# Kernel optimization log

Hardware: AMD Instinct MI355X
Metric: run time of the kernel (lower is better)

The kernel has to match this reference:

```python
import jax, jax.numpy as jnp
import numpy as np

HEAD = 4      # args.head
N_HOPS = 2    # n_hops == gt_layer


def setup_inputs() -> dict:
    key = jax.random.key(0)
    ks = jax.random.split(key, 8)
    N, D, E, R = 100000, 64, 800000, 32
    entity_emb = jax.random.normal(ks[0], (N, D), dtype=jnp.float32) * 0.1
    weight = jax.random.normal(ks[1], (R - 1, D), dtype=jnp.float32) * 0.1
    Wq = jax.random.normal(ks[2], (N_HOPS, D, D), dtype=jnp.float32) * (1.0 / np.sqrt(D))
    Wk = jax.random.normal(ks[3], (N_HOPS, D, D), dtype=jnp.float32) * (1.0 / np.sqrt(D))
    Wv = jax.random.normal(ks[4], (N_HOPS, D, D), dtype=jnp.float32) * (1.0 / np.sqrt(D))
    edge_index = jax.random.randint(ks[5], (2, E), 0, N, dtype=jnp.int64 if jax.config.jax_enable_x64 else jnp.int32)
    edge_type = jax.random.randint(ks[6], (E,), 1, R, dtype=edge_index.dtype)  # in [1, R-1]
    return {"entity_emb": entity_emb, "weight": weight, "Wq": Wq, "Wk": Wk,
            "Wv": Wv, "edge_index": edge_index, "edge_type": edge_type}


def _kg_layer(rows, col_embeds, embeds, n_nodes, wq, wk, wv):
    # per-edge scaled-dot attention with index_add softmax normalization
    E, D = col_embeds.shape
    dh = D // HEAD
    q = (embeds[rows] @ wq).reshape(E, HEAD, dh)
    k = (col_embeds @ wk).reshape(E, HEAD, dh)
    v = (col_embeds @ wv).reshape(E, HEAD, dh)
    att = jnp.clip(jnp.einsum('ehd,ehd->eh', q, k), -10.0, 10.0)
    exp_att = jnp.exp(att)                                        # [E, H]
    att_norm = jax.ops.segment_sum(exp_att, rows, num_segments=n_nodes)[rows]
    a = exp_att / (att_norm + 1e-8)
    res = (a[..., None] * v).reshape(E, D)
    return jax.ops.segment_sum(res, rows, num_segments=n_nodes)   # [N, D]


def _scatter_softmax(x, index, n_seg):
    # numerically-stable softmax over edges grouped by index (torch_scatter.scatter_softmax)
    m = jax.ops.segment_max(x, index, num_segments=n_seg)
    e = jnp.exp(x - m[index])
    s = jax.ops.segment_sum(e, index, num_segments=n_seg)
    return e / (s[index] + 1e-16)


def reference(entity_emb, weight, Wq, Wk, Wv, edge_index, edge_type):
    N, D = entity_emb.shape
    head, tail = edge_index[0], edge_index[1]
    rel = weight[edge_type - 1]                                   # [E, D]
    emb = entity_emb
    res = entity_emb
    for layer in range(N_HOPS):
        neigh_rel = emb[tail] * rel                               # [E, D]
        kg_emb = _kg_layer(head, neigh_rel, emb, N, Wq[layer], Wk[layer], Wv[layer])
        # calculate_sim_hrt: product of L2 norms, squared (scalar per edge)
        hn = jnp.linalg.norm(kg_emb[head] * rel, axis=1)
        tn = jnp.linalg.norm(kg_emb[tail] * rel, axis=1)
        w = (hn * tn) ** 2                                        # [E]
        a = _scatter_softmax(w, head, N)                          # [E]
        neigh = a[:, None] * emb[tail]                            # [E, D]
        agg = jax.ops.segment_sum(neigh, head, num_segments=N)    # [N, D]
        # F.normalize + residual accumulation across hops
        emb = agg / jnp.maximum(jnp.linalg.norm(agg, axis=1, keepdims=True), 1e-12)
        res = res + emb
    return res
```

## Files before the change

kernel.cpp:

```cpp
#include <hip/hip_runtime.h>
#include <hip/hip_fp16.h>
#include <math.h>

#define BD 256
#define CAP 192
#define PBLK 2048

#define RED16(v) { v += __shfl_xor(v, 1, 64); v += __shfl_xor(v, 2, 64); \
                   v += __shfl_xor(v, 4, 64); v += __shfl_xor(v, 8, 64); }
#define REDQ(v)  { v += __shfl_xor(v, 16, 64); v += __shfl_xor(v, 32, 64); }

__device__ __forceinline__ __half2 shflxor_h2(__half2 v, int off) {
  int i = __shfl_xor(*(int*)&v, off, 64);
  return *(__half2*)&i;
}
#define REDQH(v)  { v = __hadd2(v, shflxor_h2(v, 16)); v = __hadd2(v, shflxor_h2(v, 32)); }
#define RED16H(v) { v = __hadd2(v, shflxor_h2(v, 1)); v = __hadd2(v, shflxor_h2(v, 2)); \
                    v = __hadd2(v, shflxor_h2(v, 4)); v = __hadd2(v, shflxor_h2(v, 8)); }

__global__ void k_init(const float4* __restrict__ ent, float4* __restrict__ emb,
                       float4* __restrict__ out, int n4, int* __restrict__ deg, int N) {
  int i = blockIdx.x * BD + threadIdx.x;
  if (i < n4) { float4 v = ent[i]; emb[i] = v; out[i] = v; }
  if (i < N) deg[i] = 0;
}

__global__ void k_deg(const int* __restrict__ head, int* __restrict__ deg, int E) {
  int e = blockIdx.x * BD + threadIdx.x;
  if (e < E) atomicAdd(&deg[head[e]], 1);
}

__global__ void k_scan_a(const int* __restrict__ deg, int* __restrict__ rowptr,
                         int* __restrict__ bsum, int N) {
  __shared__ int s[BD];
  int t = threadIdx.x, i = blockIdx.x * BD + t;
  int v = (i < N) ? deg[i] : 0;
  s[t] = v; __syncthreads();
  for (int off = 1; off < BD; off <<= 1) {
    int add = (t >= off) ? s[t - off] : 0;
    __syncthreads();
    s[t] += add;
    __syncthreads();
  }
  if (i < N) rowptr[i] = s[t] - v;
  if (t == BD - 1) bsum[blockIdx.x] = s[t];
}

__global__ void k_scan_b(const int* __restrict__ bsum, int* __restrict__ boff, int nb) {
  __shared__ int s[512];
  int t = threadIdx.x;
  int v = (t < nb) ? bsum[t] : 0;
  s[t] = v; __syncthreads();
  for (int off = 1; off < 512; off <<= 1) {
    int add = (t >= off) ? s[t - off] : 0;
    __syncthreads();
    s[t] += add;
    __syncthreads();
  }
  boff[t] = s[t] - v;
}

__global__ void k_scan_c(int* __restrict__ rowptr, int* __restrict__ cur,
                         const int* __restrict__ boff, int N, int E) {
  int i = blockIdx.x * BD + threadIdx.x;
  if (i < N) { int v = rowptr[i] + boff[blockIdx.x]; rowptr[i] = v; cur[i] = v; }
  if (i == 0) rowptr[N] = E;
}

__global__ void k_scatter(const int* __restrict__ head, const int* __restrict__ tail,
                          const int* __restrict__ etype,
                          int* __restrict__ cur, int2* __restrict__ epack, int E) {
  int e = blockIdx.x * BD + threadIdx.x;
  if (e < E) {
    int p = atomicAdd(&cur[head[e]], 1);
    epack[p] = make_int2(tail[e], etype[e] - 1);
  }
}

__global__ void k_m(const float* __restrict__ Wq, const float* __restrict__ Wk,
                    float* __restrict__ Mf) {
  int tid = blockIdx.x * BD + threadIdx.x;
  int c = tid & 255;
  int m = tid >> 8;
  int i = c >> 2, h = c & 3;
  const float* wq = Wq + m * 64 + h * 16;
  const float* wk = Wk + i * 64 + h * 16;
  float acc = 0.f;
#pragma unroll
  for (int d = 0; d < 16; d++) acc = fmaf(wq[d], wk[d], acc);
  Mf[tid] = acc;
}

__global__ __launch_bounds__(256) void k_g(const float* __restrict__ emb,
                                           const float* __restrict__ Mf,
                                           uint2* __restrict__ Gh2, int N) {
  __shared__ float lM[64 * 256];
  int t = threadIdx.x;
  const float4* Mf4 = (const float4*)Mf;
  float4* lM4 = (float4*)lM;
  for (int i = t; i < 4096; i += BD) lM4[i] = Mf4[i];
  __syncthreads();
  int lane = t & 63, w = t >> 6;
  int nloc0 = blockIdx.x * 64 + w * 16;
#pragma unroll
  for (int b = 0; b < 2; b++) {
    int nl = nloc0 + b * 8;
    float4 acc[8];
#pragma unroll
    for (int ni = 0; ni < 8; ni++) acc[ni] = make_float4(0.f, 0.f, 0.f, 0.f);
#pragma unroll 8
    for (int m = 0; m < 64; m++) {
      float4 Mv = lM4[m * 64 + lane];
#pragma unroll
      for (int ni = 0; ni < 8; ni++) {
        float em = emb[(size_t)(nl + ni) * 64 + m];
        acc[ni].x = fmaf(em, Mv.x, acc[ni].x);
        acc[ni].y = fmaf(em, Mv.y, acc[ni].y);
        acc[ni].z = fmaf(em, Mv.z, acc[ni].z);
        acc[ni].w = fmaf(em, Mv.w, acc[ni].w);
      }
    }
#pragma unroll
    for (int ni = 0; ni < 8; ni++)
      if (nl + ni < N) {
        __half2 h01 = __floats2half2_rn(acc[ni].x, acc[ni].y);
        __half2 h23 = __floats2half2_rn(acc[ni].z, acc[ni].w);
        uint2 st;
        st.x = *(unsigned int*)&h01;
        st.y = *(unsigned int*)&h23;
        Gh2[(size_t)(nl + ni) * 64 + lane] = st;
      }
  }
}

__global__ __launch_bounds__(256) void k_fused(const float* __restrict__ emb,
                        const float* __restrict__ weight,
                        const uint4* __restrict__ Ghq, const float* __restrict__ Wv,
                        const int2* __restrict__ epack, const int* __restrict__ rowptr,
                        float* __restrict__ kg, int N) {
  __shared__ float SL[4 * 272];
  int t = threadIdx.x, lane = t & 63, w = t >> 6, q = lane >> 4, s = lane & 15;
  float* L = SL + w * 272;
  int wid = blockIdx.x * 4 + w, nw = gridDim.x * 4;
  const __half2 z2 = __float2half2_rn(0.f);
  for (int n = wid; n < N; n += nw) {
    uint4 ga = Ghq[(size_t)n * 32 + s * 2];
    uint4 gb = Ghq[(size_t)n * 32 + s * 2 + 1];
    __half2 c0h01 = *(__half2*)&ga.x, c0h23 = *(__half2*)&ga.y;
    __half2 c1h01 = *(__half2*)&ga.z, c1h23 = *(__half2*)&ga.w;
    __half2 c2h01 = *(__half2*)&gb.x, c2h23 = *(__half2*)&gb.y;
    __half2 c3h01 = *(__half2*)&gb.z, c3h23 = *(__half2*)&gb.w;

    int base = rowptr[n], deg = rowptr[n + 1] - base;
    float4 den = make_float4(0.f, 0.f, 0.f, 0.f);
    __half2 S0a = z2, S0b = z2, S1a = z2, S1b = z2;
    __half2 S2a = z2, S2b = z2, S3a = z2, S3b = z2;
    for (int g0 = 0; g0 < deg; g0 += 4) {
      int k = g0 + q;
      bool valid = (k < deg);
      int kk = min(k, deg - 1);
      int2 p = epack[base + kk];
      float4 e4 = *(const float4*)(emb + (size_t)p.x * 64 + s * 4);
      float4 r4 = *(const float4*)(weight + (size_t)p.y * 64 + s * 4);
      __half2 x01 = __floats2half2_rn(e4.x * r4.x, e4.y * r4.y);
      __half2 x23 = __floats2half2_rn(e4.z * r4.z, e4.w * r4.w);
      __half2 b0 = __low2half2(x01), b1 = __high2half2(x01);
      __half2 b2 = __low2half2(x23), b3 = __high2half2(x23);
      __half2 a01 = __hmul2(b0, c0h01);
      a01 = __hfma2(b1, c1h01, a01);
      a01 = __hfma2(b2, c2h01, a01);
      a01 = __hfma2(b3, c3h01, a01);
      __half2 a23 = __hmul2(b0, c0h23);
      a23 = __hfma2(b1, c1h23, a23);
      a23 = __hfma2(b2, c2h23, a23);
      a23 = __hfma2(b3, c3h23, a23);
      RED16H(a01) RED16H(a23)
      float2 fa01 = __half22float2(a01);
      float2 fa23 = __half22float2(a23);
      fa01.x = fminf(10.f, fmaxf(-10.f, fa01.x));
      fa01.y = fminf(10.f, fmaxf(-10.f, fa01.y));
      fa23.x = fminf(10.f, fmaxf(-10.f, fa23.x));
      fa23.y = fminf(10.f, fmaxf(-10.f, fa23.y));
      float4 ev;
      ev.x = valid ? __expf(fa01.x) : 0.f;
      ev.y = valid ? __expf(fa01.y) : 0.f;
      ev.z = valid ? __expf(fa23.x) : 0.f;
      ev.w = valid ? __expf(fa23.y) : 0.f;
      den.x += ev.x; den.y += ev.y; den.z += ev.z; den.w += ev.w;
      __half2 e01 = __floats2half2_rn(ev.x, ev.y);
      __half2 e23 = __floats2half2_rn(ev.z, ev.w);
      S0a = __hfma2(e01, b0, S0a); S0b = __hfma2(e23, b0, S0b);
      S1a = __hfma2(e01, b1, S1a); S1b = __hfma2(e23, b1, S1b);
      S2a = __hfma2(e01, b2, S2a); S2b = __hfma2(e23, b2, S2b);
      S3a = __hfma2(e01, b3, S3a); S3b = __hfma2(e23, b3, S3b);
    }
    REDQ(den.x) REDQ(den.y) REDQ(den.z) REDQ(den.w)
    REDQH(S0a) REDQH(S0b) REDQH(S1a) REDQH(S1b)
    REDQH(S2a) REDQH(S2b) REDQH(S3a) REDQH(S3b)
    float4 inv;
    inv.x = 1.f / (den.x + 1e-8f); inv.y = 1.f / (den.y + 1e-8f);
    inv.z = 1.f / (den.z + 1e-8f); inv.w = 1.f / (den.w + 1e-8f);
    float2 c0, c1;
    c0 = __half22float2(S0a); c1 = __half22float2(S0b);
    float s0h0 = c0.x * inv.x, s0h1 = c0.y * inv.y, s0h2 = c1.x * inv.z, s0h3 = c1.y * inv.w;
    c0 = __half22float2(S1a); c1 = __half22float2(S1b);
    float s1h0 = c0.x * inv.x, s1h1 = c0.y * inv.y, s1h2 = c1.x * inv.z, s1h3 = c1.y * inv.w;
    c0 = __half22float2(S2a); c1 = __half22float2(S2b);
    float s2h0 = c0.x * inv.x, s2h1 = c0.y * inv.y, s2h2 = c1.x * inv.z, s2h3 = c1.y * inv.w;
    c0 = __half22float2(S3a); c1 = __half22float2(S3b);
    float s3h0 = c0.x * inv.x, s3h1 = c0.y * inv.y, s3h2 = c1.x * inv.z, s3h3 = c1.y * inv.w;
    if (q == 0) {
      *(float4*)(L +       s * 4) = make_float4(s0h0, s1h0, s2h0, s3h0);
      *(float4*)(L +  68 + s * 4) = make_float4(s0h1, s1h1, s2h1, s3h1);
      *(float4*)(L + 136 + s * 4) = make_float4(s0h2, s1h2, s2h2, s3h2);
      *(float4*)(L + 204 + s * 4) = make_float4(s0h3, s1h3, s2h3, s3h3);
    }
    const float4* L4 = (const float4*)(L + q * 68);
    float acc = 0.f;
#pragma unroll
    for (int i4 = 0; i4 < 16; i4++) {
      float4 Lv = L4[i4];
      acc = fmaf(Lv.x, Wv[(i4 * 4 + 0) * 64 + lane], acc);
      acc = fmaf(Lv.y, Wv[(i4 * 4 + 1) * 64 + lane], acc);
      acc = fmaf(Lv.z, Wv[(i4 * 4 + 2) * 64 + lane], acc);
      acc = fmaf(Lv.w, Wv[(i4 * 4 + 3) * 64 + lane], acc);
    }
    kg[(size_t)n * 64 + lane] = acc;
  }
}

__global__ __launch_bounds__(256) void k_d(const float4* __restrict__ kg4,
                    const float* __restrict__ weight,
                    float* __restrict__ D, int N) {
  __shared__ float R2T[64 * 32];
  __shared__ float KG2[64 * 68];
  int t = threadIdx.x;
  for (int i = t; i < 2048; i += BD) {
    int j = i >> 5, r = i & 31;
    float v = (r < 31) ? weight[r * 64 + j] : 0.f;
    R2T[i] = v * v;
  }
  int nbase = blockIdx.x * 64;
  const float4* src = kg4 + (size_t)nbase * 16;
#pragma unroll
  for (int i = 0; i < 4; i++) {
    int idx = t + i * 256;
    float4 v = src[idx];
    float* dst = KG2 + (idx >> 4) * 68 + (idx & 15) * 4;
    dst[0] = v.x * v.x; dst[1] = v.y * v.y; dst[2] = v.z * v.z; dst[3] = v.w * v.w;
  }
  __syncthreads();
  int r = t & 31, ng = t >> 5;
  float acc[8] = {0.f, 0.f, 0.f, 0.f, 0.f, 0.f, 0.f, 0.f};
  const float* kbase = KG2 + ng * 8 * 68;
#pragma unroll 4
  for (int j4 = 0; j4 < 16; j4++) {
    float r0 = R2T[(j4 * 4 + 0) * 32 + r];
    float r1 = R2T[(j4 * 4 + 1) * 32 + r];
    float r2 = R2T[(j4 * 4 + 2) * 32 + r];
    float r3 = R2T[(j4 * 4 + 3) * 32 + r];
#pragma unroll
    for (int ni = 0; ni < 8; ni++) {
      float4 kv = *(const float4*)(kbase + ni * 68 + j4 * 4);
      acc[ni] = fmaf(kv.w, r3, fmaf(kv.z, r2, fmaf(kv.y, r1, fmaf(kv.x, r0, acc[ni]))));
    }
  }
  if (r < 31) {
    int nlim = N - nbase;
#pragma unroll
    for (int ni = 0; ni < 8; ni++) {
      int nl = ng * 8 + ni;
      if (nl < nlim) D[(size_t)(nbase + nl) * 32 + r] = acc[ni];
    }
  }
}

__global__ __launch_bounds__(256) void k_aggnorm(const float* __restrict__ emb,
                          const float* __restrict__ D,
                          const int2* __restrict__ epack, const int* __restrict__ rowptr,
                          float* __restrict__ embn, float* __restrict__ out, int N) {
  __shared__ float wls[4 * CAP];
  __shared__ float DnL[4 * 32];
  int t = threadIdx.x, lane = t & 63, w = t >> 6, q = lane >> 4, s = lane & 15;
  float* wl = wls + w * CAP;
  float* Dn = DnL + w * 32;
  int wid = blockIdx.x * 4 + w, nw = gridDim.x * 4;
  for (int n = wid; n < N; n += nw) {
    int base = rowptr[n], deg = rowptr[n + 1] - base;
    if (lane < 32) Dn[lane] = (lane < 31) ? D[(size_t)n * 32 + lane] : 0.f;
    float4 agg = make_float4(0.f, 0.f, 0.f, 0.f);
    float sacc = 0.f;
    float m = -1e30f;
    if (deg > 0) {
      for (int k = lane; k < deg; k += 64) {
        int2 p = epack[base + k];
        float wv = Dn[p.y] * D[(size_t)p.x * 32 + p.y];
        if (k < CAP) wl[k] = wv;
        m = fmaxf(m, wv);
      }
#pragma unroll
      for (int off = 32; off >= 1; off >>= 1) m = fmaxf(m, __shfl_xor(m, off, 64));
      for (int g0 = 0; g0 < deg; g0 += 4) {
        int k = g0 + q;
        bool valid = (k < deg);
        int kk = min(k, deg - 1);
        int2 p = epack[base + kk];
        float4 e4 = *(const float4*)(emb + (size_t)p.x * 64 + s * 4);
        float wv = (kk < CAP) ? wl[kk] : Dn[p.y] * D[(size_t)p.x * 32 + p.y];
        float a = valid ? __expf(wv - m) : 0.f;
        sacc += a;
        agg.x = fmaf(a, e4.x, agg.x);
        agg.y = fmaf(a, e4.y, agg.y);
        agg.z = fmaf(a, e4.z, agg.z);
        agg.w = fmaf(a, e4.w, agg.w);
      }
    }
    REDQ(sacc)
    REDQ(agg.x) REDQ(agg.y) REDQ(agg.z) REDQ(agg.w)
    float sinv = 1.f / (sacc + 1e-16f);
    agg.x *= sinv; agg.y *= sinv; agg.z *= sinv; agg.w *= sinv;
    float ss = agg.x * agg.x + agg.y * agg.y + agg.z * agg.z + agg.w * agg.w;
    RED16(ss)
    float nr = fmaxf(sqrtf(ss), 1e-12f);
    float rin = 1.f / nr;
    float4 en;
    en.x = agg.x * rin; en.y = agg.y * rin; en.z = agg.z * rin; en.w = agg.w * rin;
    if (q == 0) {
      float4* eo = (float4*)(embn + (size_t)n * 64) + s;
      *eo = en;
      float4* oo = (float4*)(out + (size_t)n * 64) + s;
      float4 ov = *oo;
      ov.x += en.x; ov.y += en.y; ov.z += en.z; ov.w += en.w;
      *oo = ov;
    }
  }
}

extern "C" void kernel_launch(void* const* d_in, const int* in_sizes, int n_in,
                              void* d_out, int out_size, void* d_ws, size_t ws_size,
                              hipStream_t stream) {
  const float* ent    = (const float*)d_in[0];
  const float* weight = (const float*)d_in[1];
  const float* Wq     = (const float*)d_in[2];
  const float* Wk     = (const float*)d_in[3];
  const float* Wv     = (const float*)d_in[4];
  const int*   eidx   = (const int*)d_in[5];
  const int*   etype  = (const int*)d_in[6];
  int N = in_sizes[0] / 64;
  int E = in_sizes[6];
  const int* head = eidx;
  const int* tail = eidx + E;

  float* ws   = (float*)d_ws;
  size_t o = 0;
  float* embA = ws + o; o += (size_t)N * 64;
  float* embB = ws + o; o += (size_t)N * 64;
  float* Gbuf = ws + o; o += (size_t)N * 128;
  float* Mf   = ws + o; o += 64 * 256;
  int2* epack = (int2*)(ws + o); o += (size_t)E * 2;
  int* rowptr = (int*)(ws + o); o += N + 1;
  int* deg    = (int*)(ws + o); o += N;
  int* cur    = (int*)(ws + o); o += N;
  int* bsum   = (int*)(ws + o); o += 512;
  int* boff   = (int*)(ws + o); o += 512;
  float* Dbuf = Gbuf;

  int n4  = N * 64 / 4;
  int bl4 = (n4 + BD - 1) / BD;
  int ebl = (E + BD - 1) / BD;
  int sbl = (N + BD - 1) / BD;

  k_init<<<bl4, BD, 0, stream>>>((const float4*)ent, (float4*)embA, (float4*)d_out,
                                 n4, deg, N);
  k_deg    <<<ebl, BD, 0, stream>>>(head, deg, E);
  k_scan_a <<<sbl, BD, 0, stream>>>(deg, rowptr, bsum, N);
  k_scan_b <<<1, 512, 0, stream>>>(bsum, boff, sbl);
  k_scan_c <<<sbl, BD, 0, stream>>>(rowptr, cur, boff, N, E);
  k_scatter<<<ebl, BD, 0, stream>>>(head, tail, etype, cur, epack, E);

  float* emb = embA;
  float* alt = embB;
  for (int l = 0; l < 2; l++) {
    const float* wq = Wq + (size_t)l * 64 * 64;
    const float* wk = Wk + (size_t)l * 64 * 64;
    const float* wv = Wv + (size_t)l * 64 * 64;

    k_m<<<64, BD, 0, stream>>>(wq, wk, Mf);
    k_g<<<(N + 63) / 64, BD, 0, stream>>>(emb, Mf, (uint2*)Gbuf, N);
    k_fused<<<PBLK, BD, 0, stream>>>(emb, weight, (const uint4*)Gbuf,
                                     wv, epack, rowptr, alt, N);
    k_d<<<(N + 63) / 64, BD, 0, stream>>>((const float4*)alt, weight, Dbuf, N);
    k_aggnorm<<<PBLK, BD, 0, stream>>>(emb, Dbuf, epack, rowptr,
                                       alt, (float*)d_out, N);
    float* tmp = emb; emb = alt; alt = tmp;
  }
}
```

Before: 615.8 us.

## Fuse per-node D computation into k_fused epilogue and store D as fp16

Removes the separate k_d kernel: k_fused now squares its kg output in shared memory and multiplies it by a precomputed squared-relation table (R2T, built once by a new kernel) to produce the 32 per-relation norms directly. The kg intermediate is never written to global memory, and D is stored as half precision, halving the random gathers of D in k_aggnorm. The costs are extra per-node work and global R2T reads inside k_fused, plus reduced precision of D, which feeds an exponent in the softmax and could shift accuracy.

After: 629.6 us. 1.02x slower.

```diff
diff --git a/kernel.cpp b/kernel.cpp
--- a/kernel.cpp
+++ b/kernel.cpp
@@ -77,6 +77,15 @@
   }
 }
 
+__global__ void k_r2t(const float* __restrict__ weight, float* __restrict__ R2T) {
+  int i = blockIdx.x * BD + threadIdx.x;
+  if (i < 2048) {
+    int j = i >> 5, r = i & 31;
+    float v = (r < 31) ? weight[r * 64 + j] : 0.f;
+    R2T[i] = v * v;
+  }
+}
+
 __global__ void k_m(const float* __restrict__ Wq, const float* __restrict__ Wk,
                     float* __restrict__ Mf) {
   int tid = blockIdx.x * BD + threadIdx.x;
@@ -136,8 +145,9 @@
 __global__ __launch_bounds__(256) void k_fused(const float* __restrict__ emb,
                         const float* __restrict__ weight,
                         const uint4* __restrict__ Ghq, const float* __restrict__ Wv,
+                        const float* __restrict__ R2T,
                         const int2* __restrict__ epack, const int* __restrict__ rowptr,
-                        float* __restrict__ kg, int N) {
+                        __half* __restrict__ D16, int N) {
   __shared__ float SL[4 * 272];
   int t = threadIdx.x, lane = t & 63, w = t >> 6, q = lane >> 4, s = lane & 15;
   float* L = SL + w * 272;
@@ -225,58 +235,23 @@
       acc = fmaf(Lv.z, Wv[(i4 * 4 + 2) * 64 + lane], acc);
       acc = fmaf(Lv.w, Wv[(i4 * 4 + 3) * 64 + lane], acc);
     }
-    kg[(size_t)n * 64 + lane] = acc;
-  }
-}
-
-__global__ __launch_bounds__(256) void k_d(const float4* __restrict__ kg4,
-                    const float* __restrict__ weight,
-                    float* __restrict__ D, int N) {
-  __shared__ float R2T[64 * 32];
-  __shared__ float KG2[64 * 68];
-  int t = threadIdx.x;
-  for (int i = t; i < 2048; i += BD) {
-    int j = i >> 5, r = i & 31;
-    float v = (r < 31) ? weight[r * 64 + j] : 0.f;
-    R2T[i] = v * v;
-  }
-  int nbase = blockIdx.x * 64;
-  const float4* src = kg4 + (size_t)nbase * 16;
-#pragma unroll
-  for (int i = 0; i < 4; i++) {
-    int idx = t + i * 256;
-    float4 v = src[idx];
-    float* dst = KG2 + (idx >> 4) * 68 + (idx & 15) * 4;
-    dst[0] = v.x * v.x; dst[1] = v.y * v.y; dst[2] = v.z * v.z; dst[3] = v.w * v.w;
-  }
-  __syncthreads();
-  int r = t & 31, ng = t >> 5;
-  float acc[8] = {0.f, 0.f, 0.f, 0.f, 0.f, 0.f, 0.f, 0.f};
-  const float* kbase = KG2 + ng * 8 * 68;
-#pragma unroll 4
-  for (int j4 = 0; j4 < 16; j4++) {
-    float r0 = R2T[(j4 * 4 + 0) * 32 + r];
-    float r1 = R2T[(j4 * 4 + 1) * 32 + r];
-    float r2 = R2T[(j4 * 4 + 2) * 32 + r];
-    float r3 = R2T[(j4 * 4 + 3) * 32 + r];
-#pragma unroll
-    for (int ni = 0; ni < 8; ni++) {
-      float4 kv = *(const float4*)(kbase + ni * 68 + j4 * 4);
-      acc[ni] = fmaf(kv.w, r3, fmaf(kv.z, r2, fmaf(kv.y, r1, fmaf(kv.x, r0, acc[ni]))));
-    }
-  }
-  if (r < 31) {
-    int nlim = N - nbase;
-#pragma unroll
-    for (int ni = 0; ni < 8; ni++) {
-      int nl = ng * 8 + ni;
-      if (nl < nlim) D[(size_t)(nbase + nl) * 32 + r] = acc[ni];
-    }
+    L[lane] = acc * acc;
+    int jh = lane >> 5;
+    const float* Kh = L + jh * 32;
+    const float* Rh = R2T + jh * 32 * 32;
+    int r = lane & 31;
+    float dacc = 0.f;
+#pragma unroll 8
+    for (int j0 = 0; j0 < 32; j0++)
+      dacc = fmaf(Kh[j0], Rh[j0 * 32 + r], dacc);
+    dacc += __shfl_xor(dacc, 32, 64);
+    if (lane < 32)
+      D16[(size_t)n * 32 + lane] = __float2half(dacc);
   }
 }
 
 __global__ __launch_bounds__(256) void k_aggnorm(const float* __restrict__ emb,
-                          const float* __restrict__ D,
+                          const __half* __restrict__ D16,
                           const int2* __restrict__ epack, const int* __restrict__ rowptr,
                           float* __restrict__ embn, float* __restrict__ out, int N) {
   __shared__ float wls[4 * CAP];
@@ -287,14 +262,14 @@
   int wid = blockIdx.x * 4 + w, nw = gridDim.x * 4;
   for (int n = wid; n < N; n += nw) {
     int base = rowptr[n], deg = rowptr[n + 1] - base;
-    if (lane < 32) Dn[lane] = (lane < 31) ? D[(size_t)n * 32 + lane] : 0.f;
+    if (lane < 32) Dn[lane] = (lane < 31) ? __half2float(D16[(size_t)n * 32 + lane]) : 0.f;
     float4 agg = make_float4(0.f, 0.f, 0.f, 0.f);
     float sacc = 0.f;
     float m = -1e30f;
     if (deg > 0) {
       for (int k = lane; k < deg; k += 64) {
         int2 p = epack[base + k];
-        float wv = Dn[p.y] * D[(size_t)p.x * 32 + p.y];
+        float wv = Dn[p.y] * __half2float(D16[(size_t)p.x * 32 + p.y]);
         if (k < CAP) wl[k] = wv;
         m = fmaxf(m, wv);
       }
@@ -306,7 +281,7 @@
         int kk = min(k, deg - 1);
         int2 p = epack[base + kk];
         float4 e4 = *(const float4*)(emb + (size_t)p.x * 64 + s * 4);
-        float wv = (kk < CAP) ? wl[kk] : Dn[p.y] * D[(size_t)p.x * 32 + p.y];
+        float wv = (kk < CAP) ? wl[kk] : Dn[p.y] * __half2float(D16[(size_t)p.x * 32 + p.y]);
         float a = valid ? __expf(wv - m) : 0.f;
         sacc += a;
         agg.x = fmaf(a, e4.x, agg.x);
@@ -357,13 +332,14 @@
   float* embB = ws + o; o += (size_t)N * 64;
   float* Gbuf = ws + o; o += (size_t)N * 128;
   float* Mf   = ws + o; o += 64 * 256;
+  float* R2T  = ws + o; o += 2048;
+  __half* D16 = (__half*)(ws + o); o += (size_t)N * 16;
   int2* epack = (int2*)(ws + o); o += (size_t)E * 2;
   int* rowptr = (int*)(ws + o); o += N + 1;
   int* deg    = (int*)(ws + o); o += N;
   int* cur    = (int*)(ws + o); o += N;
   int* bsum   = (int*)(ws + o); o += 512;
   int* boff   = (int*)(ws + o); o += 512;
-  float* Dbuf = Gbuf;
 
   int n4  = N * 64 / 4;
   int bl4 = (n4 + BD - 1) / BD;
@@ -377,6 +353,7 @@
   k_scan_b <<<1, 512, 0, stream>>>(bsum, boff, sbl);
   k_scan_c <<<sbl, BD, 0, stream>>>(rowptr, cur, boff, N, E);
   k_scatter<<<ebl, BD, 0, stream>>>(head, tail, etype, cur, epack, E);
+  k_r2t    <<<8, BD, 0, stream>>>(weight, R2T);
 
   float* emb = embA;
   float* alt = embB;
@@ -388,9 +365,8 @@
     k_m<<<64, BD, 0, stream>>>(wq, wk, Mf);
     k_g<<<(N + 63) / 64, BD, 0, stream>>>(emb, Mf, (uint2*)Gbuf, N);
     k_fused<<<PBLK, BD, 0, stream>>>(emb, weight, (const uint4*)Gbuf,
-                                     wv, epack, rowptr, alt, N);
-    k_d<<<(N + 63) / 64, BD, 0, stream>>>((const float4*)alt, weight, Dbuf, N);
-    k_aggnorm<<<PBLK, BD, 0, stream>>>(emb, Dbuf, epack, rowptr,
+                                     wv, R2T, epack, rowptr, D16, N);
+    k_aggnorm<<<PBLK, BD, 0, stream>>>(emb, D16, epack, rowptr,
                                        alt, (float*)d_out, N);
     float* tmp = emb; emb = alt; alt = tmp;
   }
```

## Store node embeddings and relation weights in fp16 to halve gather traffic

Applied to the files above, without the earlier changes.

Keeps the running node embedding in fp16 instead of fp32. k_init, k_g, k_fused and k_aggnorm now read and write half-precision rows, and a small kernel builds an fp16 copy of the relation weights. The aim is to halve the bytes moved by the random per-edge gathers of tail embeddings and relation rows, which dominate memory traffic. kg output moves to a separate buffer, and k_g now unpacks two embedding values per load. The cost is lower precision in the embeddings and in the hop-to-hop propagation, which may push the output error closer to tolerance.

New measurement: 585.3 us. -4.9%, faster.

```diff
diff --git a/kernel.cpp b/kernel.cpp
--- a/kernel.cpp
+++ b/kernel.cpp
@@ -18,10 +18,17 @@
 #define RED16H(v) { v = __hadd2(v, shflxor_h2(v, 1)); v = __hadd2(v, shflxor_h2(v, 2)); \
                     v = __hadd2(v, shflxor_h2(v, 4)); v = __hadd2(v, shflxor_h2(v, 8)); }
 
-__global__ void k_init(const float4* __restrict__ ent, float4* __restrict__ emb,
+__global__ void k_init(const float4* __restrict__ ent, uint2* __restrict__ e16,
                        float4* __restrict__ out, int n4, int* __restrict__ deg, int N) {
   int i = blockIdx.x * BD + threadIdx.x;
-  if (i < n4) { float4 v = ent[i]; emb[i] = v; out[i] = v; }
+  if (i < n4) {
+    float4 v = ent[i];
+    out[i] = v;
+    __half2 h01 = __floats2half2_rn(v.x, v.y);
+    __half2 h23 = __floats2half2_rn(v.z, v.w);
+    uint2 st; st.x = *(unsigned int*)&h01; st.y = *(unsigned int*)&h23;
+    e16[i] = st;
+  }
   if (i < N) deg[i] = 0;
 }
 
@@ -77,6 +84,14 @@
   }
 }
 
+__global__ void k_w16(const float* __restrict__ weight, __half* __restrict__ w16) {
+  int i = blockIdx.x * BD + threadIdx.x;
+  if (i < 2048) {
+    int r = i >> 6, j = i & 63;
+    w16[i] = __float2half((r < 31) ? weight[r * 64 + j] : 0.f);
+  }
+}
+
 __global__ void k_m(const float* __restrict__ Wq, const float* __restrict__ Wk,
                     float* __restrict__ Mf) {
   int tid = blockIdx.x * BD + threadIdx.x;
@@ -91,7 +106,7 @@
   Mf[tid] = acc;
 }
 
-__global__ __launch_bounds__(256) void k_g(const float* __restrict__ emb,
+__global__ __launch_bounds__(256) void k_g(const __half* __restrict__ e16,
                                            const float* __restrict__ Mf,
                                            uint2* __restrict__ Gh2, int N) {
   __shared__ float lM[64 * 256];
@@ -108,16 +123,22 @@
     float4 acc[8];
 #pragma unroll
     for (int ni = 0; ni < 8; ni++) acc[ni] = make_float4(0.f, 0.f, 0.f, 0.f);
-#pragma unroll 8
-    for (int m = 0; m < 64; m++) {
-      float4 Mv = lM4[m * 64 + lane];
+#pragma unroll 4
+    for (int m = 0; m < 64; m += 2) {
+      float4 Mv0 = lM4[m * 64 + lane];
+      float4 Mv1 = lM4[(m + 1) * 64 + lane];
 #pragma unroll
       for (int ni = 0; ni < 8; ni++) {
-        float em = emb[(size_t)(nl + ni) * 64 + m];
-        acc[ni].x = fmaf(em, Mv.x, acc[ni].x);
-        acc[ni].y = fmaf(em, Mv.y, acc[ni].y);
-        acc[ni].z = fmaf(em, Mv.z, acc[ni].z);
-        acc[ni].w = fmaf(em, Mv.w, acc[ni].w);
+        __half2 eh = *(const __half2*)(e16 + (size_t)(nl + ni) * 64 + m);
+        float2 ef = __half22float2(eh);
+        acc[ni].x = fmaf(ef.x, Mv0.x, acc[ni].x);
+        acc[ni].y = fmaf(ef.x, Mv0.y, acc[ni].y);
+        acc[ni].z = fmaf(ef.x, Mv0.z, acc[ni].z);
+        acc[ni].w = fmaf(ef.x, Mv0.w, acc[ni].w);
+        acc[ni].x = fmaf(ef.y, Mv1.x, acc[ni].x);
+        acc[ni].y = fmaf(ef.y, Mv1.y, acc[ni].y);
+        acc[ni].z = fmaf(ef.y, Mv1.z, acc[ni].z);
+        acc[ni].w = fmaf(ef.y, Mv1.w, acc[ni].w);
       }
     }
 #pragma unroll
@@ -133,8 +154,8 @@
   }
 }
 
-__global__ __launch_bounds__(256) void k_fused(const float* __restrict__ emb,
-                        const float* __restrict__ weight,
+__global__ __launch_bounds__(256) void k_fused(const uint2* __restrict__ e16,
+                        const uint2* __restrict__ w16,
                         const uint4* __restrict__ Ghq, const float* __restrict__ Wv,
                         const int2* __restrict__ epack, const int* __restrict__ rowptr,
                         float* __restrict__ kg, int N) {
@@ -160,10 +181,10 @@
       bool valid = (k < deg);
       int kk = min(k, deg - 1);
       int2 p = epack[base + kk];
-      float4 e4 = *(const float4*)(emb + (size_t)p.x * 64 + s * 4);
-      float4 r4 = *(const float4*)(weight + (size_t)p.y * 64 + s * 4);
-      __half2 x01 = __floats2half2_rn(e4.x * r4.x, e4.y * r4.y);
-      __half2 x23 = __floats2half2_rn(e4.z * r4.z, e4.w * r4.w);
+      uint2 eu = e16[(size_t)p.x * 16 + s];
+      uint2 ru = w16[(size_t)p.y * 16 + s];
+      __half2 x01 = __hmul2(*(__half2*)&eu.x, *(__half2*)&ru.x);
+      __half2 x23 = __hmul2(*(__half2*)&eu.y, *(__half2*)&ru.y);
       __half2 b0 = __low2half2(x01), b1 = __high2half2(x01);
       __half2 b2 = __low2half2(x23), b3 = __high2half2(x23);
       __half2 a01 = __hmul2(b0, c0h01);
@@ -275,10 +296,10 @@
   }
 }
 
-__global__ __launch_bounds__(256) void k_aggnorm(const float* __restrict__ emb,
+__global__ __launch_bounds__(256) void k_aggnorm(const uint2* __restrict__ e16,
                           const float* __restrict__ D,
                           const int2* __restrict__ epack, const int* __restrict__ rowptr,
-                          float* __restrict__ embn, float* __restrict__ out, int N) {
+                          uint2* __restrict__ en16, float* __restrict__ out, int N) {
   __shared__ float wls[4 * CAP];
   __shared__ float DnL[4 * 32];
   int t = threadIdx.x, lane = t & 63, w = t >> 6, q = lane >> 4, s = lane & 15;
@@ -305,14 +326,16 @@
         bool valid = (k < deg);
         int kk = min(k, deg - 1);
         int2 p = epack[base + kk];
-        float4 e4 = *(const float4*)(emb + (size_t)p.x * 64 + s * 4);
+        uint2 eu = e16[(size_t)p.x * 16 + s];
+        float2 ef0 = __half22float2(*(__half2*)&eu.x);
+        float2 ef1 = __half22float2(*(__half2*)&eu.y);
         float wv = (kk < CAP) ? wl[kk] : Dn[p.y] * D[(size_t)p.x * 32 + p.y];
         float a = valid ? __expf(wv - m) : 0.f;
         sacc += a;
-        agg.x = fmaf(a, e4.x, agg.x);
-        agg.y = fmaf(a, e4.y, agg.y);
-        agg.z = fmaf(a, e4.z, agg.z);
-        agg.w = fmaf(a, e4.w, agg.w);
+        agg.x = fmaf(a, ef0.x, agg.x);
+        agg.y = fmaf(a, ef0.y, agg.y);
+        agg.z = fmaf(a, ef1.x, agg.z);
+        agg.w = fmaf(a, ef1.y, agg.w);
       }
     }
     REDQ(sacc)
@@ -326,8 +349,10 @@
     float4 en;
     en.x = agg.x * rin; en.y = agg.y * rin; en.z = agg.z * rin; en.w = agg.w * rin;
     if (q == 0) {
-      float4* eo = (float4*)(embn + (size_t)n * 64) + s;
-      *eo = en;
+      __half2 h01 = __floats2half2_rn(en.x, en.y);
+      __half2 h23 = __floats2half2_rn(en.z, en.w);
+      uint2 st; st.x = *(unsigned int*)&h01; st.y = *(unsigned int*)&h23;
+      en16[(size_t)n * 16 + s] = st;
       float4* oo = (float4*)(out + (size_t)n * 64) + s;
       float4 ov = *oo;
       ov.x += en.x; ov.y += en.y; ov.z += en.z; ov.w += en.w;
@@ -351,47 +376,50 @@
   const int* head = eidx;
   const int* tail = eidx + E;
 
-  float* ws   = (float*)d_ws;
+  float* ws    = (float*)d_ws;
   size_t o = 0;
-  float* embA = ws + o; o += (size_t)N * 64;
-  float* embB = ws + o; o += (size_t)N * 64;
-  float* Gbuf = ws + o; o += (size_t)N * 128;
-  float* Mf   = ws + o; o += 64 * 256;
-  int2* epack = (int2*)(ws + o); o += (size_t)E * 2;
-  int* rowptr = (int*)(ws + o); o += N + 1;
-  int* deg    = (int*)(ws + o); o += N;
-  int* cur    = (int*)(ws + o); o += N;
-  int* bsum   = (int*)(ws + o); o += 512;
-  int* boff   = (int*)(ws + o); o += 512;
-  float* Dbuf = Gbuf;
+  float* e16A  = ws + o; o += (size_t)N * 32;
+  float* e16B  = ws + o; o += (size_t)N * 32;
+  float* kgbuf = ws + o; o += (size_t)N * 64;
+  float* Gbuf  = ws + o; o += (size_t)N * 128;
+  float* Mf    = ws + o; o += 64 * 256;
+  float* w16   = ws + o; o += 1024;
+  int2* epack  = (int2*)(ws + o); o += (size_t)E * 2;
+  int* rowptr  = (int*)(ws + o); o += N + 1;
+  int* deg     = (int*)(ws + o); o += N;
+  int* cur     = (int*)(ws + o); o += N;
+  int* bsum    = (int*)(ws + o); o += 512;
+  int* boff    = (int*)(ws + o); o += 512;
+  float* Dbuf  = Gbuf;
 
   int n4  = N * 64 / 4;
   int bl4 = (n4 + BD - 1) / BD;
   int ebl = (E + BD - 1) / BD;
   int sbl = (N + BD - 1) / BD;
 
-  k_init<<<bl4, BD, 0, stream>>>((const float4*)ent, (float4*)embA, (float4*)d_out,
+  k_init<<<bl4, BD, 0, stream>>>((const float4*)ent, (uint2*)e16A, (float4*)d_out,
                                  n4, deg, N);
   k_deg    <<<ebl, BD, 0, stream>>>(head, deg, E);
   k_scan_a <<<sbl, BD, 0, stream>>>(deg, rowptr, bsum, N);
   k_scan_b <<<1, 512, 0, stream>>>(bsum, boff, sbl);
   k_scan_c <<<sbl, BD, 0, stream>>>(rowptr, cur, boff, N, E);
   k_scatter<<<ebl, BD, 0, stream>>>(head, tail, etype, cur, epack, E);
-
-  float* emb = embA;
-  float* alt = embB;
+  k_w16    <<<8, BD, 0, stream>>>(weight, (__half*)w16);
+
+  float* emb = e16A;
+  float* alt = e16B;
   for (int l = 0; l < 2; l++) {
     const float* wq = Wq + (size_t)l * 64 * 64;
     const float* wk = Wk + (size_t)l * 64 * 64;
     const float* wv = Wv + (size_t)l * 64 * 64;
 
     k_m<<<64, BD, 0, stream>>>(wq, wk, Mf);
-    k_g<<<(N + 63) / 64, BD, 0, stream>>>(emb, Mf, (uint2*)Gbuf, N);
-    k_fused<<<PBLK, BD, 0, stream>>>(emb, weight, (const uint4*)Gbuf,
-                                     wv, epack, rowptr, alt, N);
-    k_d<<<(N + 63) / 64, BD, 0, stream>>>((const float4*)alt, weight, Dbuf, N);
-    k_aggnorm<<<PBLK, BD, 0, stream>>>(emb, Dbuf, epack, rowptr,
-                                       alt, (float*)d_out, N);
+    k_g<<<(N + 63) / 64, BD, 0, stream>>>((const __half*)emb, Mf, (uint2*)Gbuf, N);
+    k_fused<<<PBLK, BD, 0, stream>>>((const uint2*)emb, (const uint2*)w16,
+                                     (const uint4*)Gbuf, wv, epack, rowptr, kgbuf, N);
+    k_d<<<(N + 63) / 64, BD, 0, stream>>>((const float4*)kgbuf, weight, Dbuf, N);
+    k_aggnorm<<<PBLK, BD, 0, stream>>>((const uint2*)emb, Dbuf, epack, rowptr,
+                                       (uint2*)alt, (float*)d_out, N);
     float* tmp = emb; emb = alt; alt = tmp;
   }
 }
```
